# Performance work log

Measured on AMD Instinct MI355X. Metric: run time of the kernel, lower is better.

The kernel has to match this reference:

```python
import jax, jax.numpy as jnp
import numpy as np
from functools import partial

B, H, W, C = 16, 64, 64, 512      # images, feature H, feature W, channels
R = 256                            # raw RPN proposals per image (sorted by objectness)
N_REGIONS = 64                     # regions kept after NMS
PH, PW = 7, 7                      # pool_size (h, w)
IOU_THR = 0.4
FH, FW = H, W                      # feature_size (h, w)
NEG = -jnp.inf


def _nms_indices(roi):
    # roi: [R, 4] (x, y, w, h). Scores are descending by construction
    # (tf.reverse(tf.range(n)/n)), so greedy NMS processes rows in order.
    x, y, w, h = roi[:, 0], roi[:, 1], roi[:, 2], roi[:, 3]
    y1, x1, y2, x2 = y, x, y + h, x + w
    area = (y2 - y1) * (x2 - x1)
    ih = jnp.maximum(jnp.minimum(y2[:, None], y2[None, :]) - jnp.maximum(y1[:, None], y1[None, :]), 0.0)
    iw = jnp.maximum(jnp.minimum(x2[:, None], x2[None, :]) - jnp.maximum(x1[:, None], x1[None, :]), 0.0)
    inter = ih * iw
    union = area[:, None] + area[None, :] - inter
    iou = jnp.where(union > 0, inter / union, 0.0)  # [R, R]

    def step(keep, xs):
        i, row = xs
        suppressed = jnp.any(keep & (row > IOU_THR))
        return keep.at[i].set(~suppressed), None

    keep, _ = jax.lax.scan(step, jnp.zeros((R,), bool), (jnp.arange(R), iou))
    rank = jnp.cumsum(keep.astype(jnp.int32)) - 1
    valid = keep & (rank < N_REGIONS)
    # Unfilled slot j gets tail index R - N_REGIONS + j, which is exactly
    # tf.concat([nms, tf.range(n_roi)[size(nms) - n_regions:]], 0).
    fill = R - N_REGIONS + jnp.arange(N_REGIONS)
    idx = fill.at[jnp.where(valid, rank, N_REGIONS)].set(jnp.arange(R), mode='drop')
    return idx


def _fix_axis(mn, mx, ps, fs):
    pad = ps - (mx - mn)
    fix_min = mn < pad // 2
    fix_max = fs - mx < (1 + pad) // 2
    symmetric = (pad > 0) & ~(fix_min | fix_max)
    omin = jnp.where(symmetric, mn - pad // 2, mn)
    omax = jnp.where(symmetric, mx + (1 + pad) // 2, mx)
    omin = jnp.where((pad > 0) & fix_min, 0, omin)
    omax = jnp.where((pad > 0) & fix_min, ps, omax)
    omin = jnp.where((pad > 0) & fix_max, fs - ps, omin)
    omax = jnp.where((pad > 0) & fix_max, fs, omax)
    return omin, omax


def _clip_roi(roi):
    # roi: [B, N_REGIONS, 4] float (x, y, w, h) -> int32 clipped (x, y, w, h)
    x_min = jnp.maximum(0.0, roi[..., 0]).astype(jnp.int32)
    y_min = jnp.maximum(0.0, roi[..., 1]).astype(jnp.int32)
    x_max = jnp.minimum(float(FW), roi[..., 0] + roi[..., 2]).astype(jnp.int32)
    y_max = jnp.minimum(float(FH), roi[..., 1] + roi[..., 3]).astype(jnp.int32)
    x_min, x_max = _fix_axis(x_min, x_max, PW, FW)   # x axis uses si=1 (width)
    y_min, y_max = _fix_axis(y_min, y_max, PH, FH)   # y axis uses si=0 (height)
    return jnp.stack([x_min, y_min, x_max - x_min, y_max - y_min], axis=-1)


def _pool_one(fm, r):
    # fm: [H, W, C]; r: int32 (x, y, w, h).
    # Faithful to the traced tf.function behaviour of _pool_roi: region.shape[0]
    # is dynamic (None) so region_shape = pool_size, hence h_step = w_step = 1:
    # bins i < PH-1 are single rows y+i; the last bin spans rows [y+PH-1, y+h).
    x, y, w, h = r[0], r[1], r[2], r[3]
    ii = y + jnp.arange(PH - 1)
    jj = x + jnp.arange(PW - 1)
    rmask = (jnp.arange(H) >= y + PH - 1) & (jnp.arange(H) < y + h)
    cmask = (jnp.arange(W) >= x + PW - 1) & (jnp.arange(W) < x + w)
    block = fm[ii[:, None], jj[None, :], :]                                   # [PH-1, PW-1, C]
    col_strip = jnp.max(jnp.where(cmask[None, :, None], fm, NEG), axis=1)     # [H, C]
    corner = jnp.max(jnp.where(rmask[:, None], col_strip, NEG), axis=0)       # [C]
    row_strip = jnp.max(jnp.where(rmask[:, None, None], fm[:, jj, :], NEG), axis=0)  # [PW-1, C]
    top = jnp.concatenate([block, col_strip[ii][:, None, :]], axis=1)         # [PH-1, PW, C]
    bottom = jnp.concatenate([row_strip, corner[None, :]], axis=0)[None]      # [1, PW, C]
    return jnp.concatenate([top, bottom], axis=0)                             # [PH, PW, C]


def _forward(features, roi):
    idx = jax.vmap(_nms_indices)(roi)                           # [B, N_REGIONS]
    roi_nms = jnp.take_along_axis(roi, idx[..., None], axis=1)  # [B, N_REGIONS, 4]
    roi_clipped = _clip_roi(roi_nms)                            # int32 [B, N_REGIONS, 4]
    pooled = jax.vmap(lambda fm, rs: jax.vmap(partial(_pool_one, fm))(rs))(features, roi_clipped)
    return pooled, roi_clipped


def setup_inputs():
    key = jax.random.key(0)
    k1, k2, k3 = jax.random.split(key, 3)
    features = jax.random.normal(k1, (B, H, W, C), dtype=jnp.float32)
    xy = jax.random.uniform(k2, (B, R, 2), dtype=jnp.float32) * 60.0
    wh = jax.random.uniform(k3, (B, R, 2), dtype=jnp.float32) * 30.0 + 2.0
    roi = jnp.concatenate([xy, wh], axis=-1)
    return {"features": features, "roi": roi}


def reference(features, roi):
    return _forward(features, roi)
```

## Files before the change

kernel.cpp:

```cpp
#include <hip/hip_runtime.h>
#include <math.h>

namespace {
constexpr int kB = 16, kH = 64, kW = 64, kC = 512;
constexpr int kR = 256, kN = 64, kPH = 7, kPW = 7;
constexpr int kC4 = kC / 4;
constexpr float kIouThr = 0.4f;
constexpr size_t kPooledElems = (size_t)kB * kN * kPH * kPW * kC;
}

__device__ __forceinline__ float4 max4(float4 a, float4 b) {
    return make_float4(fmaxf(a.x, b.x), fmaxf(a.y, b.y),
                       fmaxf(a.z, b.z), fmaxf(a.w, b.w));
}

__global__ __launch_bounds__(256) void nms_clip_kernel(
        const float* __restrict__ roi, float* __restrict__ out_roi) {
    const int b = blockIdx.x;
    const int tid = threadIdx.x;
    const float* r = roi + (size_t)b * kR * 4;

    __shared__ float4 box[kR];
    __shared__ float area[kR];
    __shared__ unsigned long long M[kR][4];
    __shared__ unsigned long long kw[4];
    __shared__ int idx[kN];

    if (tid < kN) idx[tid] = kR - kN + tid;

    const float4 rr = ((const float4*)r)[tid];
    const float x1 = rr.x, y1 = rr.y, x2 = rr.x + rr.z, y2 = rr.y + rr.w;
    box[tid] = make_float4(x1, y1, x2, y2);
    area[tid] = (y2 - y1) * (x2 - x1);
    __syncthreads();

    {
        unsigned long long m0 = 0, m1 = 0, m2 = 0, m3 = 0;
        const float ai = area[tid];
        for (int j = 0; j < kR; ++j) {
            const float4 bj = box[j];
            const float ih = fmaxf(fminf(y2, bj.w) - fmaxf(y1, bj.y), 0.0f);
            const float iw = fmaxf(fminf(x2, bj.z) - fmaxf(x1, bj.x), 0.0f);
            const float inter = ih * iw;
            const float uni = ai + area[j] - inter;
            const float iou = (uni > 0.0f) ? (inter / uni) : 0.0f;
            if (iou > kIouThr) {
                const unsigned long long bit = 1ull << (j & 63);
                if ((j >> 6) == 0) m0 |= bit;
                else if ((j >> 6) == 1) m1 |= bit;
                else if ((j >> 6) == 2) m2 |= bit;
                else m3 |= bit;
            }
        }
        M[tid][0] = m0; M[tid][1] = m1; M[tid][2] = m2; M[tid][3] = m3;
    }
    __syncthreads();

    if (tid == 0) {
        unsigned long long s0 = 0, s1 = 0, s2 = 0, s3 = 0;
        unsigned long long k0 = 0, k1 = 0, k2 = 0, k3 = 0;
        unsigned long long n0 = M[0][0], n1 = M[0][1], n2 = M[0][2], n3 = M[0][3];
#pragma unroll
        for (int wi = 0; wi < 4; ++wi) {
            for (int bi = 0; bi < 64; ++bi) {
                const unsigned long long m0 = n0, m1 = n1, m2 = n2, m3 = n3;
                const int ip = (wi * 64 + bi + 1) & 255;
                n0 = M[ip][0]; n1 = M[ip][1]; n2 = M[ip][2]; n3 = M[ip][3];
                const unsigned long long sw =
                    (wi == 0) ? s0 : (wi == 1) ? s1 : (wi == 2) ? s2 : s3;
                if (!((sw >> bi) & 1ull)) {
                    const unsigned long long bit = 1ull << bi;
                    if (wi == 0) k0 |= bit;
                    else if (wi == 1) k1 |= bit;
                    else if (wi == 2) k2 |= bit;
                    else k3 |= bit;
                    s0 |= m0; s1 |= m1; s2 |= m2; s3 |= m3;
                }
            }
        }
        kw[0] = k0; kw[1] = k1; kw[2] = k2; kw[3] = k3;
    }
    __syncthreads();

    {
        const int wi = tid >> 6, bi = tid & 63;
        const unsigned long long kwv = kw[wi];
        if ((kwv >> bi) & 1ull) {
            int rank = 0;
            for (int w2 = 0; w2 < wi; ++w2) rank += __popcll(kw[w2]);
            const unsigned long long below =
                (bi == 0) ? 0ull : (~0ull >> (64 - bi));
            rank += __popcll(kwv & below);
            if (rank < kN) idx[rank] = tid;
        }
    }
    __syncthreads();

    if (tid < kN) {
        const int i = idx[tid];
        const float x = r[i * 4 + 0], y = r[i * 4 + 1];
        const float w = r[i * 4 + 2], h = r[i * 4 + 3];
        int x_min = (int)fmaxf(0.0f, x);
        int y_min = (int)fmaxf(0.0f, y);
        int x_max = (int)fminf((float)kW, x + w);
        int y_max = (int)fminf((float)kH, y + h);
        {
            const int pad = kPW - (x_max - x_min);
            const bool fmn = x_min < (pad >> 1);
            const bool fmx = (kW - x_max) < ((1 + pad) >> 1);
            const bool sym = (pad > 0) && !(fmn || fmx);
            int omin = sym ? (x_min - (pad >> 1)) : x_min;
            int omax = sym ? (x_max + ((1 + pad) >> 1)) : x_max;
            if ((pad > 0) && fmn) { omin = 0; omax = kPW; }
            if ((pad > 0) && fmx) { omin = kW - kPW; omax = kW; }
            x_min = omin; x_max = omax;
        }
        {
            const int pad = kPH - (y_max - y_min);
            const bool fmn = y_min < (pad >> 1);
            const bool fmx = (kH - y_max) < ((1 + pad) >> 1);
            const bool sym = (pad > 0) && !(fmn || fmx);
            int omin = sym ? (y_min - (pad >> 1)) : y_min;
            int omax = sym ? (y_max + ((1 + pad) >> 1)) : y_max;
            if ((pad > 0) && fmn) { omin = 0; omax = kPH; }
            if ((pad > 0) && fmx) { omin = kH - kPH; omax = kH; }
            y_min = omin; y_max = omax;
        }
        float4 rf;
        rf.x = (float)x_min; rf.y = (float)y_min;
        rf.z = (float)(x_max - x_min); rf.w = (float)(y_max - y_min);
        ((float4*)out_roi)[b * kN + tid] = rf;
    }
}

__global__ __launch_bounds__(256) void pool_kernel(
        const float4* __restrict__ fm4, const float4* __restrict__ rcf,
        float4* __restrict__ out4) {
    constexpr int kNBlk = kB * kN * 4;
    constexpr int kCpx = kNBlk / 8;
    const int bid = (blockIdx.x & 7) * kCpx + (blockIdx.x >> 3);
    const int rid = bid >> 2;
    const int q4 = bid & 3;
    const int b = rid >> 6;
    const int tid = threadIdx.x;
    const int s = tid >> 5;
    const int t = tid & 31;
    const int g = q4 * 32 + t;

    const float4 rf = rcf[rid];
    const int x = (int)rf.x, y = (int)rf.y;
    const int w = (int)rf.z, h = (int)rf.w;

    const float4* fm = fm4 + (size_t)b * kH * kW * kC4 + g;
    float4* out = out4 + (size_t)rid * (kPH * kPW) * kC4 + g;

    const float NI = -__builtin_inff();
    const float4 ninf = make_float4(NI, NI, NI, NI);

    if (s < 6) {
        const int p = s;
        const float4* row = fm + ((y + p) * kW + x) * kC4;
        float4 v0 = row[0 * kC4], v1 = row[1 * kC4], v2 = row[2 * kC4];
        float4 v3 = row[3 * kC4], v4 = row[4 * kC4], v5 = row[5 * kC4];
        out[(p * 7 + 0) * kC4] = v0;
        out[(p * 7 + 1) * kC4] = v1;
        out[(p * 7 + 2) * kC4] = v2;
        out[(p * 7 + 3) * kC4] = v3;
        out[(p * 7 + 4) * kC4] = v4;
        out[(p * 7 + 5) * kC4] = v5;
        float4 m0 = ninf, m1 = ninf, m2 = ninf, m3 = ninf;
        int j = 6;
        for (; j + 4 <= w; j += 4) {
            float4 a0 = row[(j + 0) * kC4], a1 = row[(j + 1) * kC4];
            float4 a2 = row[(j + 2) * kC4], a3 = row[(j + 3) * kC4];
            m0 = max4(m0, a0); m1 = max4(m1, a1);
            m2 = max4(m2, a2); m3 = max4(m3, a3);
        }
        for (; j < w; ++j) m0 = max4(m0, row[j * kC4]);
        out[(p * 7 + 6) * kC4] = max4(max4(m0, m1), max4(m2, m3));
    }

    float4 pm[7];
#pragma unroll
    for (int o = 0; o < 7; ++o) pm[o] = ninf;
    for (int i = y + 6 + s; i < y + h; i += 8) {
        const float4* row = fm + (i * kW + x) * kC4;
#pragma unroll
        for (int q = 0; q < 6; ++q) pm[q] = max4(pm[q], row[q * kC4]);
        float4 c0 = pm[6], c1 = ninf, c2 = ninf, c3 = ninf;
        int j = 6;
        for (; j + 4 <= w; j += 4) {
            float4 a0 = row[(j + 0) * kC4], a1 = row[(j + 1) * kC4];
            float4 a2 = row[(j + 2) * kC4], a3 = row[(j + 3) * kC4];
            c0 = max4(c0, a0); c1 = max4(c1, a1);
            c2 = max4(c2, a2); c3 = max4(c3, a3);
        }
        for (; j < w; ++j) c0 = max4(c0, row[j * kC4]);
        pm[6] = max4(max4(c0, c1), max4(c2, c3));
    }

    __shared__ float4 red[4][kPH][32];
    if (s >= 4) {
#pragma unroll
        for (int o = 0; o < 7; ++o) red[s - 4][o][t] = pm[o];
    }
    __syncthreads();
    if (s < 4) {
#pragma unroll
        for (int o = 0; o < 7; ++o) pm[o] = max4(pm[o], red[s][o][t]);
    }
    __syncthreads();
    if (s == 2 || s == 3) {
#pragma unroll
        for (int o = 0; o < 7; ++o) red[s - 2][o][t] = pm[o];
    }
    __syncthreads();
    if (s < 2) {
#pragma unroll
        for (int o = 0; o < 7; ++o) pm[o] = max4(pm[o], red[s][o][t]);
    }
    __syncthreads();
    if (s == 1) {
#pragma unroll
        for (int o = 0; o < 7; ++o) red[0][o][t] = pm[o];
    }
    __syncthreads();
    if (s == 0) {
#pragma unroll
        for (int o = 0; o < 7; ++o) {
            out[(42 + o) * kC4] = max4(pm[o], red[0][o][t]);
        }
    }
}

extern "C" void kernel_launch(void* const* d_in, const int* in_sizes, int n_in,
                              void* d_out, int out_size, void* d_ws, size_t ws_size,
                              hipStream_t stream) {
    (void)in_sizes; (void)n_in; (void)d_ws; (void)ws_size; (void)out_size;
    const float* features = (const float*)d_in[0];
    const float* roi = (const float*)d_in[1];
    float* out = (float*)d_out;
    float* out_roi = out + kPooledElems;

    nms_clip_kernel<<<kB, 256, 0, stream>>>(roi, out_roi);
    pool_kernel<<<kB * kN * 4, 256, 0, stream>>>(
        (const float4*)features, (const float4*)out_roi, (float4*)out);
}
```

Baseline: 307.3 us.

## Schedule pool blocks largest-ROI-first via per-batch area sort

The NMS/clip kernel now bitonic-sorts each image's 64 clipped regions by area in descending order and writes the resulting permutation to the workspace. The pool kernel uses that permutation to map block indices, so the biggest regions are dispatched first while the chunk-by-batch grouping for cache locality is kept. The aim is to cut tail imbalance, where a few large-ROI blocks finish last. The cost is extra sort synchronisation in the single-block-per-image NMS kernel and one more indirect load per pool block.

```diff
diff --git a/kernel.cpp b/kernel.cpp
--- a/kernel.cpp
+++ b/kernel.cpp
@@ -15,7 +15,8 @@
 }
 
 __global__ __launch_bounds__(256) void nms_clip_kernel(
-        const float* __restrict__ roi, float* __restrict__ out_roi) {
+        const float* __restrict__ roi, float* __restrict__ out_roi,
+        int* __restrict__ perm) {
     const int b = blockIdx.x;
     const int tid = threadIdx.x;
     const float* r = roi + (size_t)b * kR * 4;
@@ -25,6 +26,7 @@
     __shared__ unsigned long long M[kR][4];
     __shared__ unsigned long long kw[4];
     __shared__ int idx[kN];
+    __shared__ int skey[kN];
 
     if (tid < kN) idx[tid] = kR - kN + tid;
 
@@ -130,18 +132,38 @@
         rf.x = (float)x_min; rf.y = (float)y_min;
         rf.z = (float)(x_max - x_min); rf.w = (float)(y_max - y_min);
         ((float4*)out_roi)[b * kN + tid] = rf;
-    }
+
+        skey[tid] = (((x_max - x_min) * (y_max - y_min)) << 6) | tid;
+    }
+    __syncthreads();
+
+    for (int k = 2; k <= kN; k <<= 1) {
+        for (int j = k >> 1; j > 0; j >>= 1) {
+            if (tid < kN) {
+                const int ixj = tid ^ j;
+                if (ixj > tid) {
+                    const int a = skey[tid], c = skey[ixj];
+                    const bool up = (tid & k) == 0;
+                    if (up ? (a < c) : (a > c)) { skey[tid] = c; skey[ixj] = a; }
+                }
+            }
+            __syncthreads();
+        }
+    }
+    if (tid < kN) perm[b * kN + tid] = skey[tid] & 63;
 }
 
 __global__ __launch_bounds__(256) void pool_kernel(
         const float4* __restrict__ fm4, const float4* __restrict__ rcf,
-        float4* __restrict__ out4) {
-    constexpr int kNBlk = kB * kN * 4;
-    constexpr int kCpx = kNBlk / 8;
-    const int bid = (blockIdx.x & 7) * kCpx + (blockIdx.x >> 3);
-    const int rid = bid >> 2;
-    const int q4 = bid & 3;
-    const int b = rid >> 6;
+        const int* __restrict__ perm, float4* __restrict__ out4) {
+    const int chunk = blockIdx.x & 7;
+    const int u = blockIdx.x >> 3;
+    const int slot = u >> 2;
+    const int q4 = u & 3;
+    const int batch = chunk * 2 + (slot & 1);
+    const int rank = slot >> 1;
+    const int rid = batch * kN + perm[batch * kN + rank];
+    const int b = batch;
     const int tid = threadIdx.x;
     const int s = tid >> 5;
     const int t = tid & 31;
@@ -236,13 +258,14 @@
 extern "C" void kernel_launch(void* const* d_in, const int* in_sizes, int n_in,
                               void* d_out, int out_size, void* d_ws, size_t ws_size,
                               hipStream_t stream) {
-    (void)in_sizes; (void)n_in; (void)d_ws; (void)ws_size; (void)out_size;
+    (void)in_sizes; (void)n_in; (void)ws_size; (void)out_size;
     const float* features = (const float*)d_in[0];
     const float* roi = (const float*)d_in[1];
     float* out = (float*)d_out;
     float* out_roi = out + kPooledElems;
-
-    nms_clip_kernel<<<kB, 256, 0, stream>>>(roi, out_roi);
+    int* perm = (int*)d_ws;
+
+    nms_clip_kernel<<<kB, 256, 0, stream>>>(roi, out_roi, perm);
     pool_kernel<<<kB * kN * 4, 256, 0, stream>>>(
-        (const float4*)features, (const float4*)out_roi, (float4*)out);
-}
+        (const float4*)features, (const float4*)out_roi, perm, (float4*)out);
+}
```

New measurement: 312.8 us. No clear change (+1.8%).
